# Optimization experiments

Hardware: AMD Instinct MI355X
Metric: run time of the kernel (lower is better)

## Reference

```python
import jax, jax.numpy as jnp
import numpy as np

B, C, H, W = 8, 32, 512, 512
WS = 8
CQ = C // 4                      # 8
N = (H // WS) * (W // WS)        # 4096 windows
ED = WS * WS * C                 # 2048 embed_dim
EPS = 1e-6


def setup_inputs() -> dict:
    key = jax.random.key(0)
    ks = jax.random.split(key, 16)
    s = 0.02
    return {
        "input_x": jax.random.normal(ks[0], (B, C, H, W), jnp.float32),
        # in_conv: Conv2d(C, C//4, 1)
        "w_in": jax.random.normal(ks[1], (CQ, C), jnp.float32) * s,
        "b_in": jnp.zeros((CQ,), jnp.float32),
        # conv: Conv2d(C, C//4, 1) + LayerNorm(C//4)
        "w_conv": jax.random.normal(ks[2], (CQ, C), jnp.float32) * s,
        "b_conv": jnp.zeros((CQ,), jnp.float32),
        "ln_w": jnp.ones((CQ,), jnp.float32),
        "ln_b": jnp.zeros((CQ,), jnp.float32),
        # out_CA: Conv2d(C//4, C, 1)
        "w_ca": jax.random.normal(ks[3], (C, CQ), jnp.float32) * s,
        "b_ca": jnp.zeros((C,), jnp.float32),
        # out_SA: Conv2d(C//4, 1, 3, pad 1)
        "w_sa": jax.random.normal(ks[4], (1, CQ, 3, 3), jnp.float32) * s,
        "b_sa": jnp.zeros((1,), jnp.float32),
        # out_mask MLP: Linear(ED, ED//2), Linear(ED//2, ED)  (torch weight [out,in])
        "w_m1": jax.random.normal(ks[5], (ED // 2, ED), jnp.float32) * s,
        "b_m1": jnp.zeros((ED // 2,), jnp.float32),
        "w_m2": jax.random.normal(ks[6], (ED, ED // 2), jnp.float32) * s,
        "b_m2": jnp.zeros((ED,), jnp.float32),
    }


def _leaky(x):
    return jax.nn.leaky_relu(x, 0.1)


def _conv1x1(x, w, b):
    # x: [B,Cin,H,W], w: [Cout,Cin]
    return jnp.einsum('bchw,oc->bohw', x, w) + b[None, :, None, None]


def reference(input_x, w_in, b_in, w_conv, b_conv, ln_w, ln_b,
              w_ca, b_ca, w_sa, b_sa, w_m1, b_m1, w_m2, b_m2):
    b_, c_, h_, w_ = input_x.shape
    n_win = (h_ // WS) * (w_ // WS)

    # in_conv branch
    x = _leaky(_conv1x1(input_x, w_in, b_in))          # [B,CQ,H,W]

    # conv branch: 1x1 conv -> channels_first LayerNorm -> leaky
    x_ = _conv1x1(input_x, w_conv, b_conv)             # [B,CQ,H,W]
    u = jnp.mean(x_, axis=1, keepdims=True)
    s = jnp.mean((x_ - u) ** 2, axis=1, keepdims=True)
    x_ = (x_ - u) / jnp.sqrt(s + EPS)
    x_ = _leaky(ln_w[None, :, None, None] * x_ + ln_b[None, :, None, None])

    # channel attention: global avg pool -> 1x1 conv -> sigmoid
    pooled = jnp.mean(x_, axis=(2, 3), keepdims=True)  # [B,CQ,1,1]
    ca = jax.nn.sigmoid(_conv1x1(pooled, w_ca, b_ca))  # [B,C,1,1]

    # spatial attention: 3x3 conv -> sigmoid
    sa = jax.lax.conv_general_dilated(
        x_, w_sa, (1, 1), 'SAME',
        dimension_numbers=('NCHW', 'OIHW', 'NCHW')) + b_sa[None, :, None, None]
    sa = jax.nn.sigmoid(sa)                            # [B,1,H,W]

    # window variance + bottom-k mask
    xm = jnp.mean(x, axis=1)                           # [B,H,W]
    xw = xm.reshape(b_, h_ // WS, WS, w_ // WS, WS)
    xw = xw.transpose(0, 1, 3, 2, 4).reshape(b_, n_win, WS * WS)  # [B,N,64]
    var_x = jnp.var(xw, axis=-1, ddof=1)               # [B,N] (torch unbiased var)
    k_top = n_win // 2
    _, idx = jax.lax.top_k(-var_x, k_top)              # indices of smallest-variance windows
    mask = jnp.ones((b_, n_win), input_x.dtype)
    mask = mask.at[jnp.arange(b_)[:, None], idx].set(0.0)  # vectorized scatter

    # broadcast 0/1 mask across embed dim, then MLP (see notes re: original bug)
    m = jnp.broadcast_to(mask[:, :, None], (b_, n_win, w_m1.shape[1]))
    hdd = _leaky(jnp.einsum('bnd,ed->bne', m, w_m1) + b_m1)
    out_mask = jnp.einsum('bne,fe->bnf', hdd, w_m2) + b_m2  # [B,N,ED]

    return (out_mask, ca, sa)
```

## Files before the change

kernel.cpp:

```cpp
#include <hip/hip_runtime.h>
#include <math.h>

#define B_   8
#define C_   32
#define H_   512
#define W_   512
#define CQ_  8
#define NW_  4096
#define ED_  2048
#define EH_  1024
#define EPS_ 1e-6f

#define TW 64
#define TH 16

#define AS1 __attribute__((address_space(1)))
#define AS3 __attribute__((address_space(3)))

__device__ __forceinline__ float leaky(float x) { return x > 0.f ? x : 0.1f * x; }
__device__ __forceinline__ float sigmoidf_(float x) { return 1.f / (1.f + __expf(-x)); }

__global__ __launch_bounds__(256, 4) void pass_a(
    const float* __restrict__ x,
    const float* __restrict__ w_in, const float* __restrict__ b_in,
    const float* __restrict__ w_conv, const float* __restrict__ b_conv,
    const float* __restrict__ ln_w, const float* __restrict__ ln_b,
    float* __restrict__ xq_out,
    double* __restrict__ var_out,
    float* __restrict__ pooled_part)
{
    __shared__ float stage[2][4][TH][TW];
    __shared__ float xm_lds[TH][TW];
    __shared__ float red[4][CQ_];

    const int tid = threadIdx.x;
    const int b  = blockIdx.z;
    const int ty = blockIdx.y * TH, tx = blockIdx.x * TW;
    const int px = (tid & 15) * 4, py = tid >> 4;
    const int lane = tid & 63, wv = tid >> 6;
    const size_t plane = (size_t)H_ * W_;
    const float* xb = x + (size_t)b * C_ * plane;

    const float* gsrc[4];
#pragma unroll
    for (int i = 0; i < 4; ++i) {
        const int j = i * 64 + lane;
        const int r = j >> 4, c4 = j & 15;
        gsrc[i] = xb + (size_t)wv * plane + (size_t)(ty + r) * W_ + tx + c4 * 4;
    }

#define STAGE(bufidx, cb)                                                     \
    {                                                                         \
        _Pragma("unroll")                                                     \
        for (int i_ = 0; i_ < 4; ++i_) {                                      \
            __builtin_amdgcn_global_load_lds(                                 \
                (const AS1 unsigned int*)(gsrc[i_] + (size_t)(cb) * 4 * plane),\
                (AS3 unsigned int*)(&stage[bufidx][wv][0][0] + i_ * 256),     \
                16, 0, 0);                                                    \
        }                                                                     \
    }

    float ycv[CQ_][4], yin[CQ_][4];
#pragma unroll
    for (int q = 0; q < CQ_; ++q)
#pragma unroll
        for (int j = 0; j < 4; ++j) { ycv[q][j] = 0.f; yin[q][j] = 0.f; }

    STAGE(0, 0);
#pragma unroll
    for (int cb = 0; cb < 8; ++cb) {
        if (cb < 7) {
            STAGE((cb + 1) & 1, cb + 1);
            asm volatile("s_waitcnt vmcnt(4)" ::: "memory");
        } else {
            asm volatile("s_waitcnt vmcnt(0)" ::: "memory");
        }
        asm volatile("s_barrier" ::: "memory");
#pragma unroll
        for (int k = 0; k < 4; ++k) {
            const int c = cb * 4 + k;
            const float4 v = *reinterpret_cast<const float4*>(&stage[cb & 1][k][py][px]);
#pragma unroll
            for (int q = 0; q < CQ_; ++q) {
                const float wc = w_conv[q * C_ + c];
                const float wi = w_in[q * C_ + c];
                ycv[q][0] = fmaf(wc, v.x, ycv[q][0]);
                ycv[q][1] = fmaf(wc, v.y, ycv[q][1]);
                ycv[q][2] = fmaf(wc, v.z, ycv[q][2]);
                ycv[q][3] = fmaf(wc, v.w, ycv[q][3]);
                yin[q][0] = fmaf(wi, v.x, yin[q][0]);
                yin[q][1] = fmaf(wi, v.y, yin[q][1]);
                yin[q][2] = fmaf(wi, v.z, yin[q][2]);
                yin[q][3] = fmaf(wi, v.w, yin[q][3]);
            }
        }
        asm volatile("s_barrier" ::: "memory");
    }
#undef STAGE

#pragma unroll
    for (int q = 0; q < CQ_; ++q) {
        const float bc = b_conv[q];
#pragma unroll
        for (int j = 0; j < 4; ++j) ycv[q][j] += bc;
    }

    float ps[CQ_];
#pragma unroll
    for (int q = 0; q < CQ_; ++q) ps[q] = 0.f;

    float xmv[4];
#pragma unroll
    for (int j = 0; j < 4; ++j) {
        float u = 0.f;
#pragma unroll
        for (int q = 0; q < CQ_; ++q) u += ycv[q][j];
        u *= 0.125f;
        float s = 0.f;
#pragma unroll
        for (int q = 0; q < CQ_; ++q) { const float d = ycv[q][j] - u; s = fmaf(d, d, s); }
        s *= 0.125f;
        const float inv = 1.f / sqrtf(s + EPS_);
        float m = 0.f;
#pragma unroll
        for (int q = 0; q < CQ_; ++q) {
            const float xv = leaky(fmaf(ln_w[q], (ycv[q][j] - u) * inv, ln_b[q]));
            ycv[q][j] = xv;
            ps[q] += xv;
            m += leaky(yin[q][j] + b_in[q]);
        }
        xmv[j] = m * 0.125f;
    }

#pragma unroll
    for (int q = 0; q < CQ_; ++q) {
        *reinterpret_cast<float4*>(
            &xq_out[(((size_t)b * CQ_ + q) * H_ + (ty + py)) * W_ + tx + px]) =
            make_float4(ycv[q][0], ycv[q][1], ycv[q][2], ycv[q][3]);
    }

    *reinterpret_cast<float4*>(&xm_lds[py][px]) = make_float4(xmv[0], xmv[1], xmv[2], xmv[3]);

#pragma unroll
    for (int q = 0; q < CQ_; ++q) {
        float s = ps[q];
#pragma unroll
        for (int off = 32; off; off >>= 1) s += __shfl_xor(s, off);
        if (lane == 0) red[wv][q] = s;
    }

    __syncthreads();

    if (tid < CQ_) {
        const float s = red[0][tid] + red[1][tid] + red[2][tid] + red[3][tid];
        const int bid = (blockIdx.z * gridDim.y + blockIdx.y) * gridDim.x + blockIdx.x;
        pooled_part[bid * CQ_ + tid] = s;
    }

#pragma unroll
    for (int k = 0; k < 4; ++k) {
        const int wi = wv * 4 + k;
        const int wy = wi >> 3, wx = wi & 7;
        const double dv = (double)xm_lds[wy * 8 + (lane >> 3)][wx * 8 + (lane & 7)];
        double s = dv;
#pragma unroll
        for (int off = 32; off; off >>= 1) s += __shfl_xor(s, off);
        const double mean = s * (1.0 / 64.0);
        const double d = dv - mean;
        double s2 = d * d;
#pragma unroll
        for (int off = 32; off; off >>= 1) s2 += __shfl_xor(s2, off);
        if (lane == 0) {
            const int n = (blockIdx.y * 2 + wy) * 64 + blockIdx.x * 8 + wx;
            var_out[(size_t)b * NW_ + n] = s2 * (1.0 / 63.0);
        }
    }
}

__global__ __launch_bounds__(256) void sa_kernel(
    const float* __restrict__ xq,
    const float* __restrict__ w_sa, const float* __restrict__ b_sa,
    float* __restrict__ sa_out)
{
    __shared__ float xl[CQ_][18][72];
    const int tid = threadIdx.x;
    const int b = blockIdx.z;
    const int ty = blockIdx.y * TH, tx = blockIdx.x * TW;

    for (int idx = tid; idx < CQ_ * 18 * 18; idx += 256) {
        const int ch = idx / 324;
        const int rem = idx % 324;
        const int r = rem / 18, c4 = rem % 18;
        const int gy = ty + r - 1;
        const int gxf = tx + c4 * 4 - 4;
        float4 v = make_float4(0.f, 0.f, 0.f, 0.f);
        if (gy >= 0 && gy < H_ && gxf >= 0 && gxf < W_)
            v = *reinterpret_cast<const float4*>(
                    &xq[(((size_t)b * CQ_ + ch) * H_ + gy) * W_ + gxf]);
        *reinterpret_cast<float4*>(&xl[ch][r][c4 * 4]) = v;
    }
    __syncthreads();

    const int px = (tid & 15) * 4, py = tid >> 4;
    const float bsa = b_sa[0];
    float acc[4] = {bsa, bsa, bsa, bsa};
#pragma unroll
    for (int q = 0; q < CQ_; ++q) {
#pragma unroll
        for (int dy = 0; dy < 3; ++dy) {
            const float* r = &xl[q][py + dy][px];
            const float4 aa = *reinterpret_cast<const float4*>(r);
            const float4 bb = *reinterpret_cast<const float4*>(r + 4);
            const float4 cc = *reinterpret_cast<const float4*>(r + 8);
            const float a[12] = {aa.x, aa.y, aa.z, aa.w, bb.x, bb.y, bb.z, bb.w,
                                 cc.x, cc.y, cc.z, cc.w};
#pragma unroll
            for (int dx = 0; dx < 3; ++dx) {
                const float w = w_sa[q * 9 + dy * 3 + dx];
#pragma unroll
                for (int j = 0; j < 4; ++j) acc[j] = fmaf(w, a[j + 3 + dx], acc[j]);
            }
        }
    }
    const float4 o = make_float4(sigmoidf_(acc[0]), sigmoidf_(acc[1]),
                                 sigmoidf_(acc[2]), sigmoidf_(acc[3]));
    *reinterpret_cast<float4*>(&sa_out[((size_t)b * H_ + (ty + py)) * W_ + tx + px]) = o;
}

__global__ __launch_bounds__(256) void k2_kernel(
    const double* __restrict__ var, float* __restrict__ maskF,
    const float* __restrict__ w_m1, const float* __restrict__ b_m1,
    float* __restrict__ h1, float* __restrict__ h0,
    const float* __restrict__ pooled_part,
    const float* __restrict__ w_ca, const float* __restrict__ b_ca,
    float* __restrict__ ca_out)
{
    __shared__ double sv[NW_];
    const int bi = blockIdx.x;
    const int tid = threadIdx.x;

    if (bi < 128) {
        const int b = bi >> 4;
        const double* vb = var + (size_t)b * NW_;
        for (int j = tid; j < NW_; j += 256) sv[j] = vb[j];
        __syncthreads();
        const int i = (bi & 15) * 256 + tid;
        const double vi = sv[i];
        int cnt = 0;
#pragma unroll 4
        for (int j = 0; j < NW_; ++j) {
            const double vj = sv[j];
            cnt += (vj < vi) || (vj == vi && j < i);
        }
        maskF[(size_t)b * NW_ + i] = (cnt < NW_ / 2) ? 0.f : 1.f;
    } else if (bi < 384) {
        const int wave = tid >> 6, lane = tid & 63;
        const int e = (bi - 128) * 4 + wave;
        const float* row = w_m1 + (size_t)e * ED_;
        float s = 0.f;
#pragma unroll
        for (int k = 0; k < ED_ / 64; ++k) s += row[lane + 64 * k];
#pragma unroll
        for (int off = 32; off; off >>= 1) s += __shfl_xor(s, off);
        if (lane == 0) {
            h1[e] = leaky(s + b_m1[e]);
            h0[e] = leaky(b_m1[e]);
        }
    } else {
        float* sp = (float*)sv;
        const int bq = tid >> 2, part = tid & 3;
        const int bb = bq >> 3, q = bq & 7;
        float s = 0.f;
        for (int k = part; k < 256; k += 4) s += pooled_part[((size_t)bb * 256 + k) * CQ_ + q];
        sp[tid] = s;
        __syncthreads();
        if (tid < 64)
            sp[256 + tid] = (sp[4 * tid] + sp[4 * tid + 1] + sp[4 * tid + 2] + sp[4 * tid + 3])
                            * (1.f / ((float)H_ * (float)W_));
        __syncthreads();
        const int ob = tid >> 5, o = tid & 31;
        float acc = b_ca[o];
#pragma unroll
        for (int qq = 0; qq < CQ_; ++qq)
            acc = fmaf(w_ca[o * CQ_ + qq], sp[256 + ob * CQ_ + qq], acc);
        ca_out[tid] = sigmoidf_(acc);
    }
}

__global__ __launch_bounds__(256) void o_kernel(const float* __restrict__ w_m2,
                                                const float* __restrict__ b_m2,
                                                const float* __restrict__ h1,
                                                const float* __restrict__ h0,
                                                float* __restrict__ o1, float* __restrict__ o0)
{
    const int wave = threadIdx.x >> 6, lane = threadIdx.x & 63;
    const int f = blockIdx.x * 4 + wave;
    const float* row = w_m2 + (size_t)f * EH_;
    float s1 = 0.f, s0 = 0.f;
#pragma unroll
    for (int k = 0; k < EH_ / 64; ++k) {
        const float w = row[lane + 64 * k];
        s1 = fmaf(w, h1[lane + 64 * k], s1);
        s0 = fmaf(w, h0[lane + 64 * k], s0);
    }
#pragma unroll
    for (int off = 32; off; off >>= 1) {
        s1 += __shfl_xor(s1, off);
        s0 += __shfl_xor(s0, off);
    }
    if (lane == 0) {
        o1[f] = s1 + b_m2[f];
        o0[f] = s0 + b_m2[f];
    }
}

__global__ __launch_bounds__(256) void bcast_kernel(const float* __restrict__ maskF,
                                                    const float* __restrict__ o1,
                                                    const float* __restrict__ o0,
                                                    float* __restrict__ out)
{
    __shared__ float sm[16];
    const int t = threadIdx.x;
    const long row0 = (long)blockIdx.x * 16;
    if (t < 16) sm[t] = maskF[row0 + t];
    const float4 a1 = ((const float4*)o1)[t], b1 = ((const float4*)o1)[t + 256];
    const float4 a0 = ((const float4*)o0)[t], b0 = ((const float4*)o0)[t + 256];
    __syncthreads();
#pragma unroll
    for (int r = 0; r < 16; ++r) {
        float4* dst = (float4*)(out + (size_t)(row0 + r) * ED_);
        const bool m = sm[r] > 0.5f;
        dst[t]       = m ? a1 : a0;
        dst[t + 256] = m ? b1 : b0;
    }
}

extern "C" void kernel_launch(void* const* d_in, const int* in_sizes, int n_in,
                              void* d_out, int out_size, void* d_ws, size_t ws_size,
                              hipStream_t stream)
{
    const float* x    = (const float*)d_in[0];
    const float* w_in = (const float*)d_in[1];
    const float* b_in = (const float*)d_in[2];
    const float* w_cv = (const float*)d_in[3];
    const float* b_cv = (const float*)d_in[4];
    const float* lnw  = (const float*)d_in[5];
    const float* lnb  = (const float*)d_in[6];
    const float* w_ca = (const float*)d_in[7];
    const float* b_ca = (const float*)d_in[8];
    const float* w_sa = (const float*)d_in[9];
    const float* b_sa = (const float*)d_in[10];
    const float* w_m1 = (const float*)d_in[11];
    const float* b_m1 = (const float*)d_in[12];
    const float* w_m2 = (const float*)d_in[13];
    const float* b_m2 = (const float*)d_in[14];

    float* out_mask = (float*)d_out;
    float* ca_out   = out_mask + (size_t)B_ * NW_ * ED_;
    float* sa_out   = ca_out + (size_t)B_ * C_;

    float* xq = out_mask;

    char* ws = (char*)d_ws;
    double* var       = (double*)ws;
    float*  maskF     = (float*)(ws + (size_t)B_ * NW_ * 8);
    float*  pooled_pp = maskF + (size_t)B_ * NW_;
    float*  h1 = pooled_pp + 2048 * CQ_;
    float*  h0 = h1 + EH_;
    float*  o1 = h0 + EH_;
    float*  o0 = o1 + ED_;

    pass_a<<<dim3(W_ / TW, H_ / TH, B_), 256, 0, stream>>>(
        x, w_in, b_in, w_cv, b_cv, lnw, lnb, xq, var, pooled_pp);
    sa_kernel<<<dim3(W_ / TW, H_ / TH, B_), 256, 0, stream>>>(xq, w_sa, b_sa, sa_out);
    k2_kernel<<<385, 256, 0, stream>>>(var, maskF, w_m1, b_m1, h1, h0,
                                       pooled_pp, w_ca, b_ca, ca_out);
    o_kernel<<<ED_ / 4, 256, 0, stream>>>(w_m2, b_m2, h1, h0, o1, o0);
    bcast_kernel<<<B_ * NW_ / 16, 256, 0, stream>>>(maskF, o1, o0, out_mask);
}
```

Baseline: 333.4 us.

## Retile pass_a into full-width 8-row bands with 1024-thread blocks and triple buffering

```diff
diff --git a/kernel.cpp b/kernel.cpp
--- a/kernel.cpp
+++ b/kernel.cpp
@@ -11,16 +11,13 @@
 #define EH_  1024
 #define EPS_ 1e-6f
 
-#define TW 64
-#define TH 16
-
 #define AS1 __attribute__((address_space(1)))
 #define AS3 __attribute__((address_space(3)))
 
 __device__ __forceinline__ float leaky(float x) { return x > 0.f ? x : 0.1f * x; }
 __device__ __forceinline__ float sigmoidf_(float x) { return 1.f / (1.f + __expf(-x)); }
 
-__global__ __launch_bounds__(256, 4) void pass_a(
+__global__ __launch_bounds__(1024, 4) void pass_a(
     const float* __restrict__ x,
     const float* __restrict__ w_in, const float* __restrict__ b_in,
     const float* __restrict__ w_conv, const float* __restrict__ b_conv,
@@ -29,36 +26,22 @@
     double* __restrict__ var_out,
     float* __restrict__ pooled_part)
 {
-    __shared__ float stage[2][4][TH][TW];
-    __shared__ float xm_lds[TH][TW];
-    __shared__ float red[4][CQ_];
-
-    const int tid = threadIdx.x;
-    const int b  = blockIdx.z;
-    const int ty = blockIdx.y * TH, tx = blockIdx.x * TW;
-    const int px = (tid & 15) * 4, py = tid >> 4;
+    __shared__ float stage[3][4096];
+    __shared__ float xm[4096];
+    __shared__ float red[16][CQ_];
+
+    const int tid  = threadIdx.x;
+    const int band = blockIdx.x;
+    const int b    = blockIdx.y;
     const int lane = tid & 63, wv = tid >> 6;
     const size_t plane = (size_t)H_ * W_;
     const float* xb = x + (size_t)b * C_ * plane;
-
-    const float* gsrc[4];
-#pragma unroll
-    for (int i = 0; i < 4; ++i) {
-        const int j = i * 64 + lane;
-        const int r = j >> 4, c4 = j & 15;
-        gsrc[i] = xb + (size_t)wv * plane + (size_t)(ty + r) * W_ + tx + c4 * 4;
-    }
-
-#define STAGE(bufidx, cb)                                                     \
-    {                                                                         \
-        _Pragma("unroll")                                                     \
-        for (int i_ = 0; i_ < 4; ++i_) {                                      \
-            __builtin_amdgcn_global_load_lds(                                 \
-                (const AS1 unsigned int*)(gsrc[i_] + (size_t)(cb) * 4 * plane),\
-                (AS3 unsigned int*)(&stage[bufidx][wv][0][0] + i_ * 256),     \
-                16, 0, 0);                                                    \
-        }                                                                     \
-    }
+    const float* gw = xb + (size_t)band * (8 * W_) + wv * 256 + lane * 4;
+
+#define STAGE(buf, c)                                                          \
+    __builtin_amdgcn_global_load_lds(                                          \
+        (const AS1 unsigned int*)(gw + (size_t)(c) * plane),                   \
+        (AS3 unsigned int*)(&stage[buf][wv * 256]), 16, 0, 0);
 
     float ycv[CQ_][4], yin[CQ_][4];
 #pragma unroll
@@ -66,35 +49,32 @@
 #pragma unroll
         for (int j = 0; j < 4; ++j) { ycv[q][j] = 0.f; yin[q][j] = 0.f; }
 
-    STAGE(0, 0);
-#pragma unroll
-    for (int cb = 0; cb < 8; ++cb) {
-        if (cb < 7) {
-            STAGE((cb + 1) & 1, cb + 1);
-            asm volatile("s_waitcnt vmcnt(4)" ::: "memory");
-        } else {
-            asm volatile("s_waitcnt vmcnt(0)" ::: "memory");
-        }
+    STAGE(0, 0) STAGE(1, 1) STAGE(2, 2)
+
+#pragma unroll
+    for (int c = 0; c < C_; ++c) {
+        if (c < 30)       asm volatile("s_waitcnt vmcnt(2)" ::: "memory");
+        else if (c == 30) asm volatile("s_waitcnt vmcnt(1)" ::: "memory");
+        else              asm volatile("s_waitcnt vmcnt(0)" ::: "memory");
         asm volatile("s_barrier" ::: "memory");
-#pragma unroll
-        for (int k = 0; k < 4; ++k) {
-            const int c = cb * 4 + k;
-            const float4 v = *reinterpret_cast<const float4*>(&stage[cb & 1][k][py][px]);
-#pragma unroll
-            for (int q = 0; q < CQ_; ++q) {
-                const float wc = w_conv[q * C_ + c];
-                const float wi = w_in[q * C_ + c];
-                ycv[q][0] = fmaf(wc, v.x, ycv[q][0]);
-                ycv[q][1] = fmaf(wc, v.y, ycv[q][1]);
-                ycv[q][2] = fmaf(wc, v.z, ycv[q][2]);
-                ycv[q][3] = fmaf(wc, v.w, ycv[q][3]);
-                yin[q][0] = fmaf(wi, v.x, yin[q][0]);
-                yin[q][1] = fmaf(wi, v.y, yin[q][1]);
-                yin[q][2] = fmaf(wi, v.z, yin[q][2]);
-                yin[q][3] = fmaf(wi, v.w, yin[q][3]);
-            }
-        }
+
+        const float4 v = *reinterpret_cast<const float4*>(&stage[c % 3][tid * 4]);
+#pragma unroll
+        for (int q = 0; q < CQ_; ++q) {
+            const float wc = w_conv[q * C_ + c];
+            const float wi = w_in[q * C_ + c];
+            ycv[q][0] = fmaf(wc, v.x, ycv[q][0]);
+            ycv[q][1] = fmaf(wc, v.y, ycv[q][1]);
+            ycv[q][2] = fmaf(wc, v.z, ycv[q][2]);
+            ycv[q][3] = fmaf(wc, v.w, ycv[q][3]);
+            yin[q][0] = fmaf(wi, v.x, yin[q][0]);
+            yin[q][1] = fmaf(wi, v.y, yin[q][1]);
+            yin[q][2] = fmaf(wi, v.z, yin[q][2]);
+            yin[q][3] = fmaf(wi, v.w, yin[q][3]);
+        }
+        asm volatile("s_waitcnt lgkmcnt(0)" ::: "memory");
         asm volatile("s_barrier" ::: "memory");
+        if (c + 3 < C_) { STAGE(c % 3, c + 3) }
     }
 #undef STAGE
 
@@ -132,14 +112,16 @@
         xmv[j] = m * 0.125f;
     }
 
+    const int py = tid >> 7, px = (tid & 127) * 4;
+
 #pragma unroll
     for (int q = 0; q < CQ_; ++q) {
         *reinterpret_cast<float4*>(
-            &xq_out[(((size_t)b * CQ_ + q) * H_ + (ty + py)) * W_ + tx + px]) =
+            &xq_out[(((size_t)b * CQ_ + q) * H_ + band * 8 + py) * W_ + px]) =
             make_float4(ycv[q][0], ycv[q][1], ycv[q][2], ycv[q][3]);
     }
 
-    *reinterpret_cast<float4*>(&xm_lds[py][px]) = make_float4(xmv[0], xmv[1], xmv[2], xmv[3]);
+    *reinterpret_cast<float4*>(&xm[tid * 4]) = make_float4(xmv[0], xmv[1], xmv[2], xmv[3]);
 
 #pragma unroll
     for (int q = 0; q < CQ_; ++q) {
@@ -152,16 +134,17 @@
     __syncthreads();
 
     if (tid < CQ_) {
-        const float s = red[0][tid] + red[1][tid] + red[2][tid] + red[3][tid];
-        const int bid = (blockIdx.z * gridDim.y + blockIdx.y) * gridDim.x + blockIdx.x;
+        float s = 0.f;
+#pragma unroll
+        for (int w = 0; w < 16; ++w) s += red[w][tid];
+        const int bid = blockIdx.y * gridDim.x + blockIdx.x;
         pooled_part[bid * CQ_ + tid] = s;
     }
 
 #pragma unroll
     for (int k = 0; k < 4; ++k) {
-        const int wi = wv * 4 + k;
-        const int wy = wi >> 3, wx = wi & 7;
-        const double dv = (double)xm_lds[wy * 8 + (lane >> 3)][wx * 8 + (lane & 7)];
+        const int win = wv * 4 + k;
+        const double dv = (double)xm[(lane >> 3) * 512 + win * 8 + (lane & 7)];
         double s = dv;
 #pragma unroll
         for (int off = 32; off; off >>= 1) s += __shfl_xor(s, off);
@@ -171,7 +154,7 @@
 #pragma unroll
         for (int off = 32; off; off >>= 1) s2 += __shfl_xor(s2, off);
         if (lane == 0) {
-            const int n = (blockIdx.y * 2 + wy) * 64 + blockIdx.x * 8 + wx;
+            const int n = band * 64 + win;
             var_out[(size_t)b * NW_ + n] = s2 * (1.0 / 63.0);
         }
     }
@@ -185,7 +168,7 @@
     __shared__ float xl[CQ_][18][72];
     const int tid = threadIdx.x;
     const int b = blockIdx.z;
-    const int ty = blockIdx.y * TH, tx = blockIdx.x * TW;
+    const int ty = blockIdx.y * 16, tx = blockIdx.x * 64;
 
     for (int idx = tid; idx < CQ_ * 18 * 18; idx += 256) {
         const int ch = idx / 324;
@@ -271,7 +254,7 @@
         const int bq = tid >> 2, part = tid & 3;
         const int bb = bq >> 3, q = bq & 7;
         float s = 0.f;
-        for (int k = part; k < 256; k += 4) s += pooled_part[((size_t)bb * 256 + k) * CQ_ + q];
+        for (int k = part; k < 64; k += 4) s += pooled_part[((size_t)bb * 64 + k) * CQ_ + q];
         sp[tid] = s;
         __syncthreads();
         if (tid < 64)
@@ -365,14 +348,14 @@
     double* var       = (double*)ws;
     float*  maskF     = (float*)(ws + (size_t)B_ * NW_ * 8);
     float*  pooled_pp = maskF + (size_t)B_ * NW_;
-    float*  h1 = pooled_pp + 2048 * CQ_;
+    float*  h1 = pooled_pp + 512 * CQ_;
     float*  h0 = h1 + EH_;
     float*  o1 = h0 + EH_;
     float*  o0 = o1 + ED_;
 
-    pass_a<<<dim3(W_ / TW, H_ / TH, B_), 256, 0, stream>>>(
+    pass_a<<<dim3(64, B_), 1024, 0, stream>>>(
         x, w_in, b_in, w_cv, b_cv, lnw, lnb, xq, var, pooled_pp);
-    sa_kernel<<<dim3(W_ / TW, H_ / TH, B_), 256, 0, stream>>>(xq, w_sa, b_sa, sa_out);
+    sa_kernel<<<dim3(8, 32, B_), 256, 0, stream>>>(xq, w_sa, b_sa, sa_out);
     k2_kernel<<<385, 256, 0, stream>>>(var, maskF, w_m1, b_m1, h1, h0,
                                        pooled_pp, w_ca, b_ca, ca_out);
     o_kernel<<<ED_ / 4, 256, 0, stream>>>(w_m2, b_m2, h1, h0, o1, o0);
```

New measurement: 345.3 us. +3.6%, slower.
